# Kernel optimization log

Measured on AMD Instinct MI355X. Metric: run time of the kernel, lower is better.

Reference implementation:

```python
import jax, jax.numpy as jnp
import numpy as np


def setup_inputs() -> dict:
    key = jax.random.key(0)
    k1, k2 = jax.random.split(key)
    B, C, H, Wl, Wr = 4, 32, 80, 160, 640
    left_feature = jax.random.normal(k1, (B, C, H, Wl), dtype=jnp.float32)
    right_feature = jax.random.normal(k2, (B, C, H, Wr), dtype=jnp.float32)
    return {"left_feature": left_feature, "right_feature": right_feature, "max_disp": 48}


def reference(left_feature, right_feature, max_disp):
    # left_feature: [B, C, H, Wl]; right_feature: [B, C, H, Wr]
    B, C, H, Wl = left_feature.shape
    Wr = right_feature.shape[3]
    d = jnp.arange(max_disp)[:, None]          # [D, 1]
    x = jnp.arange(Wl)[None, :]                # [1, Wl]
    idx = jnp.clip(4 * x - d + 1, 0, Wr - 1)   # [D, Wl] clipped gather indices
    # gather along right width: [B, C, H, D, Wl] -> [B, C, D, H, Wl]
    right = right_feature[:, :, :, idx].transpose(0, 1, 3, 2, 4)
    return left_feature[:, :, None, :, :] - right
```

## Files before the change

kernel.cpp:

```cpp
#include <hip/hip_runtime.h>


constexpr int Bc  = 4;
constexpr int Cc  = 32;
constexpr int Hc  = 80;
constexpr int WLc = 160;
constexpr int WRc = 640;
constexpr int TPB = 256;
constexpr int GROUPS = WLc / 4;

__global__ __launch_bounds__(TPB) void diffvol_kernel(
    const float* __restrict__ left, const float* __restrict__ right,
    float* __restrict__ out, int D)
{
    __shared__ __align__(16) float lrow[WLc];
    __shared__ float rrow[WRc + WRc / 32];

    const int blk = blockIdx.x;
    const int h   = blk % Hc;
    const int bc  = blk / Hc;

    const float* lp = left  + ((size_t)bc * Hc + h) * WLc;
    const float* rp = right + ((size_t)bc * Hc + h) * WRc;

    const int tid = threadIdx.x;
    if (tid < WLc) lrow[tid] = lp[tid];
    for (int i = tid; i < WRc; i += TPB) rrow[i + (i >> 5)] = rp[i];
    __syncthreads();

    float* ob = out + ((size_t)bc * D * Hc + h) * WLc;

    const int total = D * GROUPS;
    for (int t = tid; t < total; t += TPB) {
        const int d  = t / GROUPS;
        const int g  = t - d * GROUPS;
        const int x0 = g * 4;

        const float4 lv = *(const float4*)(lrow + x0);
        float4 v;
        float* vp = (float*)&v;
        const float* lvp = (const float*)&lv;
        #pragma unroll
        for (int j = 0; j < 4; ++j) {
            int r = 4 * (x0 + j) - d + 1;
            r = r < 0 ? 0 : r;
            vp[j] = lvp[j] - rrow[r + (r >> 5)];
        }
        *(float4*)(ob + (size_t)d * (Hc * WLc) + x0) = v;
    }
}

extern "C" void kernel_launch(void* const* d_in, const int* in_sizes, int n_in,
                              void* d_out, int out_size, void* d_ws, size_t ws_size,
                              hipStream_t stream) {
    const float* left  = (const float*)d_in[0];
    const float* right = (const float*)d_in[1];
    float* out = (float*)d_out;

    const int D = out_size / (Bc * Cc * Hc * WLc);

    dim3 grid(Bc * Cc * Hc);
    diffvol_kernel<<<grid, TPB, 0, stream>>>(left, right, out, D);
}
```

Baseline: 72.49 us.

## Process eight rows per block with per-thread disparity loop and vectorized loads

Each block now handles eight H rows with 320 threads. Each thread owns one float4 of the left row and loops over all disparities, so the per-element divide is gone and the left value is reused across all D. Loads from global memory use float4 and are scattered into a padded shared-memory layout. The disparity count is specialised at compile time for 48. In exchange the grid has fewer, larger blocks and uses more shared memory per block, and each wave's store pattern changes.

```diff
diff --git a/kernel.cpp b/kernel.cpp
--- a/kernel.cpp
+++ b/kernel.cpp
@@ -6,47 +6,71 @@
 constexpr int Hc  = 80;
 constexpr int WLc = 160;
 constexpr int WRc = 640;
-constexpr int TPB = 256;
-constexpr int GROUPS = WLc / 4;
+constexpr int HB  = 8;
+constexpr int TPB = HB * (WLc / 4);
+constexpr int RPAD = WRc + WRc / 32;
 
+template<int DFIX>
 __global__ __launch_bounds__(TPB) void diffvol_kernel(
     const float* __restrict__ left, const float* __restrict__ right,
-    float* __restrict__ out, int D)
+    float* __restrict__ out, int Ddyn)
 {
-    __shared__ __align__(16) float lrow[WLc];
-    __shared__ float rrow[WRc + WRc / 32];
+    const int D = DFIX ? DFIX : Ddyn;
 
+    __shared__ __align__(16) float lrow[HB * WLc];
+    __shared__ float rrow[HB * RPAD];
+
+    constexpr int NHB = Hc / HB;
     const int blk = blockIdx.x;
-    const int h   = blk % Hc;
-    const int bc  = blk / Hc;
+    const int hb  = blk % NHB;
+    const int bc  = blk / NHB;
+    const int h0  = hb * HB;
 
-    const float* lp = left  + ((size_t)bc * Hc + h) * WLc;
-    const float* rp = right + ((size_t)bc * Hc + h) * WRc;
+    const float* lp = left  + ((size_t)bc * Hc + h0) * WLc;
+    const float* rp = right + ((size_t)bc * Hc + h0) * WRc;
 
     const int tid = threadIdx.x;
-    if (tid < WLc) lrow[tid] = lp[tid];
-    for (int i = tid; i < WRc; i += TPB) rrow[i + (i >> 5)] = rp[i];
+
+    {
+        float4 v = *(const float4*)(lp + tid * 4);
+        *(float4*)(lrow + tid * 4) = v;
+    }
+    #pragma unroll
+    for (int it = 0; it < (HB * WRc / 4) / TPB; ++it) {
+        int i   = tid + it * TPB;
+        int row = i / (WRc / 4);
+        int c4  = (i - row * (WRc / 4)) * 4;
+        float4 v = *(const float4*)(rp + row * WRc + c4);
+        float* dst = rrow + row * RPAD;
+        const float* vv = (const float*)&v;
+        #pragma unroll
+        for (int k = 0; k < 4; ++k) {
+            int c = c4 + k;
+            dst[c + (c >> 5)] = vv[k];
+        }
+    }
     __syncthreads();
 
-    float* ob = out + ((size_t)bc * D * Hc + h) * WLc;
+    const int hl = tid / (WLc / 4);
+    const int g  = tid - hl * (WLc / 4);
+    const float4 lv = *(const float4*)(lrow + tid * 4);
+    const float* rb = rrow + hl * RPAD;
+    const int r0 = 16 * g + 1;
 
-    const int total = D * GROUPS;
-    for (int t = tid; t < total; t += TPB) {
-        const int d  = t / GROUPS;
-        const int g  = t - d * GROUPS;
-        const int x0 = g * 4;
+    float* ob = out + (size_t)bc * D * (Hc * WLc) + h0 * WLc + tid * 4;
+    const float* lvp = (const float*)&lv;
 
-        const float4 lv = *(const float4*)(lrow + x0);
+    #pragma unroll 4
+    for (int d = 0; d < D; ++d) {
         float4 v;
         float* vp = (float*)&v;
-        const float* lvp = (const float*)&lv;
         #pragma unroll
         for (int j = 0; j < 4; ++j) {
-            int r = 4 * (x0 + j) - d + 1;
-            r = r < 0 ? 0 : r;
-            vp[j] = lvp[j] - rrow[r + (r >> 5)];
+            int c = r0 + 4 * j - d;
+            c = c < 0 ? 0 : c;
+            vp[j] = lvp[j] - rb[c + (c >> 5)];
         }
-        *(float4*)(ob + (size_t)d * (Hc * WLc) + x0) = v;
+        *(float4*)(ob + (size_t)d * (Hc * WLc)) = v;
     }
 }
 
@@ -59,6 +83,10 @@
 
     const int D = out_size / (Bc * Cc * Hc * WLc);
 
-    dim3 grid(Bc * Cc * Hc);
-    diffvol_kernel<<<grid, TPB, 0, stream>>>(left, right, out, D);
+    dim3 grid(Bc * Cc * (Hc / HB));
+    if (D == 48) {
+        diffvol_kernel<48><<<grid, TPB, 0, stream>>>(left, right, out, D);
+    } else {
+        diffvol_kernel<0><<<grid, TPB, 0, stream>>>(left, right, out, D);
+    }
 }
```

Result: slower. 117.5 us (+62.0%).

## Add D=48 specialized kernel processing four rows per block with vectorized loads

Applied to the files above, without the earlier changes.

Adds a kernel specialized for 48 disparities in which each block handles four image rows with 320 threads. Each thread owns one float4 column group and loops over half the disparities, so its left values stay in registers and the per-element index divide goes away. Global loads into shared memory now use float4. The cost is a dispatch on D and fewer, larger blocks (2560 instead of 10240), which changes occupancy and how the writes are spread.

```diff
diff --git a/kernel.cpp b/kernel.cpp
--- a/kernel.cpp
+++ b/kernel.cpp
@@ -6,36 +6,96 @@
 constexpr int Hc  = 80;
 constexpr int WLc = 160;
 constexpr int WRc = 640;
-constexpr int TPB = 256;
-constexpr int GROUPS = WLc / 4;
+constexpr int RPAD = WRc + WRc / 32;
 
-__global__ __launch_bounds__(TPB) void diffvol_kernel(
+constexpr int HB   = 4;
+constexpr int NHB  = Hc / HB;
+constexpr int TPB4 = 320;
+
+__global__ __launch_bounds__(TPB4) void diffvol48(
+    const float* __restrict__ left, const float* __restrict__ right,
+    float* __restrict__ out)
+{
+    constexpr int D = 48;
+    __shared__ __align__(16) float lrow[HB * WLc];
+    __shared__ float rrow[HB * RPAD];
+
+    const int blk = blockIdx.x;
+    const int hb  = blk % NHB;
+    const int bc  = blk / NHB;
+    const int h0  = hb * HB;
+
+    const float* lp = left  + ((size_t)bc * Hc + h0) * WLc;
+    const float* rp = right + ((size_t)bc * Hc + h0) * WRc;
+    const int tid = threadIdx.x;
+
+    if (tid < HB * WLc / 4)
+        *(float4*)(lrow + tid * 4) = *(const float4*)(lp + tid * 4);
+    #pragma unroll
+    for (int it = 0; it < 2; ++it) {
+        int i   = tid + it * TPB4;
+        int row = i / (WRc / 4);
+        int c4  = (i - row * (WRc / 4)) * 4;
+        float4 v = *(const float4*)(rp + row * WRc + c4);
+        float* dst = rrow + row * RPAD;
+        const float* vv = (const float*)&v;
+        #pragma unroll
+        for (int k = 0; k < 4; ++k) { int c = c4 + k; dst[c + (c >> 5)] = vv[k]; }
+    }
+    __syncthreads();
+
+    const int dp = tid / 160;
+    const int m  = tid - dp * 160;
+    const int hl = m / 40;
+    const int g  = m - hl * 40;
+
+    const float4 lv  = *(const float4*)(lrow + m * 4);
+    const float* lvp = (const float*)&lv;
+    const float* rb  = rrow + hl * RPAD;
+    int e = 16 * g + 1 - dp;
+    float* op = out + (size_t)bc * (D * Hc * WLc) + (size_t)dp * (Hc * WLc)
+                    + h0 * WLc + m * 4;
+
+    #pragma unroll 6
+    for (int k = 0; k < D / 2; ++k) {
+        float4 v; float* vp = (float*)&v;
+        #pragma unroll
+        for (int j = 0; j < 4; ++j) {
+            int c = e + 4 * j;
+            c = c < 0 ? 0 : c;
+            vp[j] = lvp[j] - rb[c + (c >> 5)];
+        }
+        *(float4*)op = v;
+        e -= 2;
+        op += 2 * (Hc * WLc);
+    }
+}
+
+constexpr int TPBG = 256;
+__global__ __launch_bounds__(TPBG) void diffvol_generic(
     const float* __restrict__ left, const float* __restrict__ right,
     float* __restrict__ out, int D)
 {
     __shared__ __align__(16) float lrow[WLc];
-    __shared__ float rrow[WRc + WRc / 32];
+    __shared__ float rrow[RPAD];
 
     const int blk = blockIdx.x;
     const int h   = blk % Hc;
     const int bc  = blk / Hc;
-
     const float* lp = left  + ((size_t)bc * Hc + h) * WLc;
     const float* rp = right + ((size_t)bc * Hc + h) * WRc;
+    const int tid = threadIdx.x;
 
-    const int tid = threadIdx.x;
     if (tid < WLc) lrow[tid] = lp[tid];
-    for (int i = tid; i < WRc; i += TPB) rrow[i + (i >> 5)] = rp[i];
+    for (int i = tid; i < WRc; i += TPBG) rrow[i + (i >> 5)] = rp[i];
     __syncthreads();
 
     float* ob = out + ((size_t)bc * D * Hc + h) * WLc;
-
-    const int total = D * GROUPS;
-    for (int t = tid; t < total; t += TPB) {
-        const int d  = t / GROUPS;
-        const int g  = t - d * GROUPS;
+    const int total = D * (WLc / 4);
+    for (int t = tid; t < total; t += TPBG) {
+        const int d  = t / (WLc / 4);
+        const int g  = t - d * (WLc / 4);
         const int x0 = g * 4;
-
         const float4 lv = *(const float4*)(lrow + x0);
         float4 v;
         float* vp = (float*)&v;
@@ -59,6 +119,11 @@
 
     const int D = out_size / (Bc * Cc * Hc * WLc);
 
-    dim3 grid(Bc * Cc * Hc);
-    diffvol_kernel<<<grid, TPB, 0, stream>>>(left, right, out, D);
+    if (D == 48) {
+        dim3 grid(Bc * Cc * NHB);
+        diffvol48<<<grid, TPB4, 0, stream>>>(left, right, out);
+    } else {
+        dim3 grid(Bc * Cc * Hc);
+        diffvol_generic<<<grid, TPBG, 0, stream>>>(left, right, out, D);
+    }
 }
```

After: 71.94 us. Within noise of the previous version (-0.8%).

## Add dense D=48 kernel with flat thread mapping and nontemporal stores

Applied to the files above, without the earlier changes.

Adds a specialized kernel for max_disp 48 in which each thread computes one float4 output and then steps through 16 (b,c) slices. Left and right values are read straight from global memory without staging in shared memory, and output goes out through nontemporal stores. The aim is to remove the shared-memory staging and barrier and to lay writes out contiguously across the grid. The generic kernel also switches to nontemporal stores. The risk is repeated uncoalesced gathers of the right row from global/L2 instead of LDS.

```diff
diff --git a/kernel.cpp b/kernel.cpp
--- a/kernel.cpp
+++ b/kernel.cpp
@@ -1,52 +1,95 @@
 #include <hip/hip_runtime.h>
 
+
+typedef float fx4 __attribute__((ext_vector_type(4)));
 
 constexpr int Bc  = 4;
 constexpr int Cc  = 32;
 constexpr int Hc  = 80;
 constexpr int WLc = 160;
 constexpr int WRc = 640;
-constexpr int TPB = 256;
+
+constexpr int Dc      = 48;
+constexpr int PLANE4  = Hc * WLc / 4;
+constexpr int BCVOL4  = Dc * PLANE4;
+constexpr int TOTAL4  = Bc * Cc * BCVOL4;
+constexpr int TPB     = 256;
+constexpr int STRIDE4 = 8 * BCVOL4;
+constexpr int NBLK    = STRIDE4 / TPB;
+constexpr int NITER   = TOTAL4 / STRIDE4;
+
+__global__ __launch_bounds__(TPB) void diffvol48_dense(
+    const float* __restrict__ left, const float* __restrict__ right,
+    float* __restrict__ out)
+{
+    const int gid = blockIdx.x * TPB + threadIdx.x;
+
+    const int x4  = gid % 40;
+    const int r1  = gid / 40;
+    const int h   = r1 % Hc;
+    const int r2  = r1 / Hc;
+    const int d   = r2 % Dc;
+    const int bc0 = r2 / Dc;
+
+    int c0 = 16 * x4 + 1 - d;
+    int rofs[4];
+    #pragma unroll
+    for (int j = 0; j < 4; ++j) { int c = c0 + 4 * j; rofs[j] = c < 0 ? 0 : c; }
+
+    const float* lptr = left  + (size_t)bc0 * (Hc * WLc) + h * WLc + x4 * 4;
+    const float* rptr = right + (size_t)bc0 * (Hc * WRc) + h * WRc;
+    float*       optr = out   + (size_t)gid * 4;
+
+    #pragma unroll 4
+    for (int k = 0; k < NITER; ++k) {
+        const fx4 lv = *(const fx4*)lptr;
+        fx4 v;
+        #pragma unroll
+        for (int j = 0; j < 4; ++j)
+            v[j] = lv[j] - rptr[rofs[j]];
+        __builtin_nontemporal_store(v, (fx4*)optr);
+
+        lptr += 8 * (Hc * WLc);
+        rptr += 8 * (Hc * WRc);
+        optr += (size_t)STRIDE4 * 4;
+    }
+}
+
 constexpr int GROUPS = WLc / 4;
-
-__global__ __launch_bounds__(TPB) void diffvol_kernel(
+constexpr int RPAD = WRc + WRc / 32;
+__global__ __launch_bounds__(TPB) void diffvol_generic(
     const float* __restrict__ left, const float* __restrict__ right,
     float* __restrict__ out, int D)
 {
     __shared__ __align__(16) float lrow[WLc];
-    __shared__ float rrow[WRc + WRc / 32];
+    __shared__ float rrow[RPAD];
 
     const int blk = blockIdx.x;
     const int h   = blk % Hc;
     const int bc  = blk / Hc;
-
     const float* lp = left  + ((size_t)bc * Hc + h) * WLc;
     const float* rp = right + ((size_t)bc * Hc + h) * WRc;
+    const int tid = threadIdx.x;
 
-    const int tid = threadIdx.x;
     if (tid < WLc) lrow[tid] = lp[tid];
     for (int i = tid; i < WRc; i += TPB) rrow[i + (i >> 5)] = rp[i];
     __syncthreads();
 
     float* ob = out + ((size_t)bc * D * Hc + h) * WLc;
-
     const int total = D * GROUPS;
     for (int t = tid; t < total; t += TPB) {
         const int d  = t / GROUPS;
         const int g  = t - d * GROUPS;
         const int x0 = g * 4;
-
-        const float4 lv = *(const float4*)(lrow + x0);
-        float4 v;
-        float* vp = (float*)&v;
-        const float* lvp = (const float*)&lv;
+        const fx4 lv = *(const fx4*)(lrow + x0);
+        fx4 v;
         #pragma unroll
         for (int j = 0; j < 4; ++j) {
             int r = 4 * (x0 + j) - d + 1;
             r = r < 0 ? 0 : r;
-            vp[j] = lvp[j] - rrow[r + (r >> 5)];
+            v[j] = lv[j] - rrow[r + (r >> 5)];
         }
-        *(float4*)(ob + (size_t)d * (Hc * WLc) + x0) = v;
+        __builtin_nontemporal_store(v, (fx4*)(ob + (size_t)d * (Hc * WLc) + x0));
     }
 }
 
@@ -59,6 +102,10 @@
 
     const int D = out_size / (Bc * Cc * Hc * WLc);
 
-    dim3 grid(Bc * Cc * Hc);
-    diffvol_kernel<<<grid, TPB, 0, stream>>>(left, right, out, D);
+    if (D == 48) {
+        diffvol48_dense<<<dim3(NBLK), TPB, 0, stream>>>(left, right, out);
+    } else {
+        dim3 grid(Bc * Cc * Hc);
+        diffvol_generic<<<grid, TPB, 0, stream>>>(left, right, out, D);
+    }
 }
```

Measured after the change: 167.2 us. 2.31x slower.
